# Optimization experiments

Measured on AMD Instinct MI355X. Metric: run time of the kernel, lower is better.

The kernel has to match this reference:

```python
import jax, jax.numpy as jnp
import numpy as np

B, S, H = 128, 512, 1024
SEP = 2


def setup_inputs() -> dict:
    key = jax.random.key(0)
    k1, k2, k3, k4 = jax.random.split(key, 4)
    hidden_states = jax.random.normal(k1, (B, S, H), dtype=jnp.float32)
    # per-sample segment boundaries: <s> title </s></s> lead </s> pad...
    title_end = jax.random.randint(k2, (B,), 5, 200)          # pos of first </s>
    lead_end = jax.random.randint(k3, (B,), 250, S - 2)        # pos of third </s>
    tokens = jax.random.randint(k4, (B, S), 5, 64000)          # avoid SEP=2 collisions
    rows = jnp.arange(B)
    input_ids = tokens.at[:, 0].set(0)                          # <s>
    input_ids = input_ids.at[rows, title_end].set(SEP)
    input_ids = input_ids.at[rows, title_end + 1].set(SEP)
    input_ids = input_ids.at[rows, lead_end].set(SEP)
    attention_mask = (jnp.arange(S)[None, :] <= lead_end[:, None]).astype(jnp.int32)
    return {
        "hidden_states": hidden_states,
        "input_ids": input_ids.astype(jnp.int64),
        "attention_mask": attention_mask,
        "sep_token_id": SEP,
    }


def reference(hidden_states, input_ids, attention_mask, sep_token_id):
    # hidden_states: (B,S,H); input_ids, attention_mask: (B,S)
    b, s, h = hidden_states.shape
    sep = input_ids == sep_token_id                      # (B,S) bool
    cnt = jnp.cumsum(sep.astype(jnp.int32), axis=1)      # inclusive sep count
    num_seps = cnt[:, -1]                                # (B,)

    def pos_of(k):
        # index of k-th separator (argmax of first True); 0 if absent
        return jnp.argmax(sep & (cnt == k), axis=1)

    p1, p2, p3 = pos_of(1), pos_of(2), pos_of(3)
    mask_len = attention_mask.sum(axis=1)
    lead_end = jnp.where(num_seps >= 3, p3, mask_len)    # (B,)
    lead_start = p2 + 1

    idx = jnp.arange(s)[None, :]                         # (1,S)
    valid = (num_seps >= 2)[:, None]
    title_mask = (idx >= 1) & (idx < p1[:, None]) & valid
    lead_mask = (idx >= lead_start[:, None]) & (idx < lead_end[:, None]) & valid

    cls = hidden_states[:, 0, :]                         # fallback: <s> token

    def masked_mean(m):
        mf = m.astype(hidden_states.dtype)               # (B,S)
        ssum = jnp.einsum('bs,bsh->bh', mf, hidden_states)
        c = mf.sum(axis=1, keepdims=True)                # (B,1)
        return jnp.where(c > 0, ssum / jnp.maximum(c, 1.0), cls)

    return masked_mean(title_mask), masked_mean(lead_mask)
```

## Files before the change

### kernel.cpp

```cpp
#include <hip/hip_runtime.h>

#define BB 128
#define SS 512
#define HH 1024
#define NB 16

typedef float f32x4 __attribute__((ext_vector_type(4)));

__device__ __forceinline__ int4 compute_meta(const int* __restrict__ ids,
                                             const int* __restrict__ attn,
                                             int b, int sep) {
    __shared__ unsigned long long words[SS / 64];
    __shared__ int sh_p[4];
    __shared__ int sh_mask;
    const int t = threadIdx.x;
    const int* row = ids + b * SS;
    const int tok0 = row[t];
    const int tok1 = row[t + 256];
    const unsigned long long b0 = __ballot(tok0 == sep);
    const unsigned long long b1 = __ballot(tok1 == sep);
    if ((t & 63) == 0) {
        words[t >> 6] = b0;
        words[4 + (t >> 6)] = b1;
    }
    if (t == 0) sh_mask = 0;
    __syncthreads();
    if (t == 0) {
        int cnt = 0, p1 = 0, p2 = 0, p3 = 0;
        for (int i = 0; i < SS / 64; ++i) {
            unsigned long long word = words[i];
            while (word && cnt < 3) {
                const int pos = i * 64 + __builtin_ctzll(word);
                ++cnt;
                if (cnt == 1) p1 = pos;
                else if (cnt == 2) p2 = pos;
                else p3 = pos;
                word &= word - 1;
            }
        }
        sh_p[0] = p1; sh_p[1] = p2; sh_p[2] = p3; sh_p[3] = cnt;
    }
    __syncthreads();
    const int cnt = sh_p[3];
    if (cnt < 3) {
        const int* arow = attn + b * SS;
        atomicAdd(&sh_mask, arow[t] + arow[t + 256]);
        __syncthreads();
    }
    int4 m;
    if (cnt >= 2) {
        m.x = 1;
        m.y = max(sh_p[0], 1);
        m.z = sh_p[1] + 1;
        const int e = (cnt >= 3) ? sh_p[2] : sh_mask;
        m.w = max(e, m.z);
    } else {
        m.x = 0; m.y = 0; m.z = 0; m.w = 0;
    }
    return m;
}

__device__ __forceinline__ int lead_first_u(int t_len, int nb) {
    int d = nb - (t_len % NB);
    if (d < 0) d += NB;
    return t_len + d;
}

__global__ void seg_sum_balanced(const float* __restrict__ hs,
                                 const int* __restrict__ ids,
                                 const int* __restrict__ attn,
                                 const int* __restrict__ sep_tok,
                                 float* __restrict__ partials) {
    const int nb = blockIdx.x;
    const int b  = blockIdx.y;
    const int4 m = compute_meta(ids, attn, b, sep_tok[0]);
    const int t_len = m.y - m.x;
    const int l_len = m.w - m.z;
    const int T = t_len + l_len;

    const int h4 = threadIdx.x;
    const f32x4* base = (const f32x4*)(hs + (size_t)b * SS * HH);
    f32x4* p = (f32x4*)(partials + (size_t)(b * NB + nb) * 2 * HH);

    if (nb < t_len) {
        f32x4 a = {0.f, 0.f, 0.f, 0.f};
        #pragma unroll 2
        for (int u = nb; u < t_len; u += NB) {
            const int s = m.x + u;
            a += __builtin_nontemporal_load(&base[(size_t)s * (HH / 4) + h4]);
        }
        p[h4] = a;
    }
    const int u0 = lead_first_u(t_len, nb);
    if (u0 < T) {
        f32x4 a = {0.f, 0.f, 0.f, 0.f};
        #pragma unroll 2
        for (int u = u0; u < T; u += NB) {
            const int s = m.z + (u - t_len);
            a += __builtin_nontemporal_load(&base[(size_t)s * (HH / 4) + h4]);
        }
        p[HH / 4 + h4] = a;
    }
}

__global__ void seg_final_balanced(const float* __restrict__ hs,
                                   const int* __restrict__ ids,
                                   const int* __restrict__ attn,
                                   const int* __restrict__ sep_tok,
                                   const float* __restrict__ partials,
                                   float* __restrict__ out) {
    const int span = blockIdx.x;
    const int b = blockIdx.y;
    const int4 m = compute_meta(ids, attn, b, sep_tok[0]);
    const int h4 = threadIdx.x;
    const int t_len = m.y - m.x;
    const int l_len = m.w - m.z;
    const int T = t_len + l_len;

    f32x4 a = {0.f, 0.f, 0.f, 0.f};
    int cntr;
    if (span == 0) {
        cntr = t_len;
        const int lim = min(t_len, NB);
        for (int nb = 0; nb < lim; ++nb) {
            const f32x4* p = (const f32x4*)(partials + (size_t)(b * NB + nb) * 2 * HH);
            a += p[h4];
        }
    } else {
        cntr = l_len;
        #pragma unroll
        for (int nb = 0; nb < NB; ++nb) {
            if (lead_first_u(t_len, nb) < T) {
                const f32x4* p = (const f32x4*)(partials + (size_t)(b * NB + nb) * 2 * HH);
                a += p[HH / 4 + h4];
            }
        }
    }

    f32x4 o;
    if (cntr > 0) {
        const float c = (float)cntr;
        o = a / c;
    } else {
        o = ((const f32x4*)(hs + (size_t)b * SS * HH))[h4];
    }
    ((f32x4*)out)[(size_t)(span * BB + b) * (HH / 4) + h4] = o;
}

extern "C" void kernel_launch(void* const* d_in, const int* in_sizes, int n_in,
                              void* d_out, int out_size, void* d_ws, size_t ws_size,
                              hipStream_t stream) {
    const float* hs  = (const float*)d_in[0];
    const int*   ids = (const int*)d_in[1];
    const int*   am  = (const int*)d_in[2];
    const int*   sep = (const int*)d_in[3];
    float* out = (float*)d_out;
    float* partials = (float*)d_ws;

    seg_sum_balanced<<<dim3(NB, BB), 256, 0, stream>>>(hs, ids, am, sep, partials);
    seg_final_balanced<<<dim3(2, BB), 256, 0, stream>>>(hs, ids, am, sep, partials, out);
}
```

Baseline: 53.64 us.

## Split segment rows into contiguous chunks per block instead of strided interleave

```diff
diff --git a/kernel.cpp b/kernel.cpp
--- a/kernel.cpp
+++ b/kernel.cpp
@@ -60,44 +60,42 @@
     return m;
 }
 
-__device__ __forceinline__ int lead_first_u(int t_len, int nb) {
-    int d = nb - (t_len % NB);
-    if (d < 0) d += NB;
-    return t_len + d;
-}
-
 __global__ void seg_sum_balanced(const float* __restrict__ hs,
                                  const int* __restrict__ ids,
                                  const int* __restrict__ attn,
                                  const int* __restrict__ sep_tok,
                                  float* __restrict__ partials) {
-    const int nb = blockIdx.x;
-    const int b  = blockIdx.y;
+    const int b  = blockIdx.x;
+    const int nb = blockIdx.y;
     const int4 m = compute_meta(ids, attn, b, sep_tok[0]);
     const int t_len = m.y - m.x;
     const int l_len = m.w - m.z;
     const int T = t_len + l_len;
 
+    const int u0 = (nb * T) / NB;
+    const int u1 = ((nb + 1) * T) / NB;
+
     const int h4 = threadIdx.x;
     const f32x4* base = (const f32x4*)(hs + (size_t)b * SS * HH);
     f32x4* p = (f32x4*)(partials + (size_t)(b * NB + nb) * 2 * HH);
 
-    if (nb < t_len) {
+    const int tA = u0, tB = min(u1, t_len);
+    if (tA < tB) {
         f32x4 a = {0.f, 0.f, 0.f, 0.f};
-        #pragma unroll 2
-        for (int u = nb; u < t_len; u += NB) {
+        #pragma unroll 4
+        for (int u = tA; u < tB; ++u) {
             const int s = m.x + u;
-            a += __builtin_nontemporal_load(&base[(size_t)s * (HH / 4) + h4]);
+            a += base[(size_t)s * (HH / 4) + h4];
         }
         p[h4] = a;
     }
-    const int u0 = lead_first_u(t_len, nb);
-    if (u0 < T) {
+    const int lA = max(u0, t_len), lB = u1;
+    if (lA < lB) {
         f32x4 a = {0.f, 0.f, 0.f, 0.f};
-        #pragma unroll 2
-        for (int u = u0; u < T; u += NB) {
+        #pragma unroll 4
+        for (int u = lA; u < lB; ++u) {
             const int s = m.z + (u - t_len);
-            a += __builtin_nontemporal_load(&base[(size_t)s * (HH / 4) + h4]);
+            a += base[(size_t)s * (HH / 4) + h4];
         }
         p[HH / 4 + h4] = a;
     }
@@ -118,29 +116,25 @@
     const int T = t_len + l_len;
 
     f32x4 a = {0.f, 0.f, 0.f, 0.f};
-    int cntr;
-    if (span == 0) {
-        cntr = t_len;
-        const int lim = min(t_len, NB);
-        for (int nb = 0; nb < lim; ++nb) {
-            const f32x4* p = (const f32x4*)(partials + (size_t)(b * NB + nb) * 2 * HH);
+    const int cntr = (span == 0) ? t_len : l_len;
+
+    #pragma unroll
+    for (int nb = 0; nb < NB; ++nb) {
+        const int u0 = (nb * T) / NB;
+        const int u1 = ((nb + 1) * T) / NB;
+        bool valid;
+        if (span == 0) valid = u0 < min(u1, t_len);
+        else           valid = max(u0, t_len) < u1;
+        if (valid) {
+            const f32x4* p = (const f32x4*)(partials +
+                (size_t)(b * NB + nb) * 2 * HH + (size_t)span * HH);
             a += p[h4];
-        }
-    } else {
-        cntr = l_len;
-        #pragma unroll
-        for (int nb = 0; nb < NB; ++nb) {
-            if (lead_first_u(t_len, nb) < T) {
-                const f32x4* p = (const f32x4*)(partials + (size_t)(b * NB + nb) * 2 * HH);
-                a += p[HH / 4 + h4];
-            }
         }
     }
 
     f32x4 o;
     if (cntr > 0) {
-        const float c = (float)cntr;
-        o = a / c;
+        o = a / (float)cntr;
     } else {
         o = ((const f32x4*)(hs + (size_t)b * SS * HH))[h4];
     }
@@ -157,6 +151,6 @@
     float* out = (float*)d_out;
     float* partials = (float*)d_ws;
 
-    seg_sum_balanced<<<dim3(NB, BB), 256, 0, stream>>>(hs, ids, am, sep, partials);
+    seg_sum_balanced<<<dim3(BB, NB), 256, 0, stream>>>(hs, ids, am, sep, partials);
     seg_final_balanced<<<dim3(2, BB), 256, 0, stream>>>(hs, ids, am, sep, partials, out);
 }
```

New measurement: 44.10 us, median of 2. -17.8%, faster.
